# Optimization experiments

Hardware: AMD Instinct MI355X
Metric: run time of the kernel (lower is better)

Reference implementation:

```python
import jax, jax.numpy as jnp
import numpy as np
from jax import lax

V = 50000      # vocab_size; pad token id == V
E = 100        # embedding dim (hard-coded in module)
H = 512        # args.hidden
T = 200        # hard-coded sequence length
B = 256        # batch
NUM_CLASSES = 5


def setup_inputs() -> dict:
    key = jax.random.key(0)
    ks = jax.random.split(key, 10)
    X = jax.random.randint(ks[0], (B, T), 0, V + 1)  # values in [0, V]; V is pad
    emb = jax.random.normal(ks[1], (V + 1, E), jnp.float32) * 0.02
    def lstm_params(k, din):
        k1, k2, k3 = jax.random.split(k, 3)
        W_ih = jax.random.normal(k1, (4 * H, din), jnp.float32) * (1.0 / np.sqrt(din))
        W_hh = jax.random.normal(k2, (4 * H, H), jnp.float32) * (1.0 / np.sqrt(H))
        b = jax.random.uniform(k3, (4 * H,), jnp.float32, -0.05, 0.05)  # b_ih+b_hh fused
        return W_ih, W_hh, b
    W_ih0, W_hh0, b0 = lstm_params(ks[2], E)
    W_ih1, W_hh1, b1 = lstm_params(ks[3], H)
    W_out = jax.random.normal(ks[4], (NUM_CLASSES, H), jnp.float32) * (1.0 / np.sqrt(H))
    b_out = jnp.zeros((NUM_CLASSES,), jnp.float32)
    return {"X": X, "emb": emb, "W_ih0": W_ih0, "W_hh0": W_hh0, "b0": b0,
            "W_ih1": W_ih1, "W_hh1": W_hh1, "b1": b1, "W_out": W_out, "b_out": b_out}


def _lstm_layer(xs, W_ih, W_hh, b):
    # xs: [T, B, din] time-major; PyTorch gate order i, f, g, o
    Bsz = xs.shape[1]
    h0 = jnp.zeros((Bsz, H), xs.dtype)
    c0 = jnp.zeros((Bsz, H), xs.dtype)
    def step(carry, x_t):
        h, c = carry
        g = x_t @ W_ih.T + h @ W_hh.T + b          # [B, 4H]
        i, f, gg, o = jnp.split(g, 4, axis=-1)
        c = jax.nn.sigmoid(f) * c + jax.nn.sigmoid(i) * jnp.tanh(gg)
        h = jax.nn.sigmoid(o) * jnp.tanh(c)
        return (h, c), h
    (_, _), hs = lax.scan(step, (h0, c0), xs)
    return hs  # [T, B, H]


def reference(X, emb, W_ih0, W_hh0, b0, W_ih1, W_hh1, b1, W_out, b_out):
    x = emb[X]                                    # [B, T, E]
    xs = jnp.swapaxes(x, 0, 1)                    # [T, B, E] time-major
    hs = _lstm_layer(xs, W_ih0, W_hh0, b0)        # [T, B, H]
    hs = _lstm_layer(hs, W_ih1, W_hh1, b1)        # [T, B, H]
    out_seq = jnp.swapaxes(hs, 0, 1)              # [B, T, H]
    # last non-pad position per row (scan-from-end in the torch loop)
    pos = jnp.arange(T)
    nonpad = X != V                               # [B, T]
    last = jnp.max(jnp.where(nonpad, pos[None, :], -1), axis=1)  # [B]
    valid = pos[None, :] <= last[:, None]         # positions 0..last inclusive
    # take_output == 'maxpooling': max over output[:, :last+1, :]
    neg = jnp.finfo(out_seq.dtype).min
    pooled = jnp.max(jnp.where(valid[:, :, None], out_seq, neg), axis=1)  # [B, H]
    logits = pooled @ W_out.T + b_out             # [B, 5]
    return logits
```

## Files before the change

kernel.cpp:

```cpp
#include <hip/hip_runtime.h>
#include <float.h>

#define V 50000
#define E 100
#define H 512
#define T 200
#define B 256
#define NC 5
#define K0 640
#define K1 1024
#define NH (B * H)
#define NW0 (2048 * K0)
#define NW1 (2048 * K1)
#define LOSC 4096.0f
#define ILOSC (1.0f / 4096.0f)

typedef _Float16 half8 __attribute__((ext_vector_type(8)));
typedef float floatx4 __attribute__((ext_vector_type(4)));

__device__ __forceinline__ float fsig(float x)  { return 1.f / (1.f + __expf(-x)); }
__device__ __forceinline__ float ftanh(float x) { return 1.f - 2.f / (__expf(2.f * x) + 1.f); }

struct WS {
    _Float16 *W0h, *W0l, *W1h, *W1l;
    _Float16 *h0h, *h0l, *h1h, *h1l;
    float *c0, *c1, *hmax;
    int *last;
};
__device__ __host__ inline WS wsmap(char* p) {
    WS w;
    w.W0h = (_Float16*)p;  p += (size_t)NW0 * 2;
    w.W0l = (_Float16*)p;  p += (size_t)NW0 * 2;
    w.W1h = (_Float16*)p;  p += (size_t)NW1 * 2;
    w.W1l = (_Float16*)p;  p += (size_t)NW1 * 2;
    w.h0h = (_Float16*)p;  p += (size_t)2 * NH * 2;
    w.h0l = (_Float16*)p;  p += (size_t)2 * NH * 2;
    w.h1h = (_Float16*)p;  p += (size_t)2 * NH * 2;
    w.h1l = (_Float16*)p;  p += (size_t)2 * NH * 2;
    w.c0   = (float*)p;    p += (size_t)NH * 4;
    w.c1   = (float*)p;    p += (size_t)NH * 4;
    w.hmax = (float*)p;    p += (size_t)NH * 4;
    w.last = (int*)p;
    return w;
}

__global__ void k_prep(const float* __restrict__ Wih0, const float* __restrict__ Whh0,
                       const float* __restrict__ Wih1, const float* __restrict__ Whh1,
                       char* wsraw) {
    WS w = wsmap(wsraw);
    int idx = blockIdx.x * 256 + threadIdx.x;
    if (idx < NW0) {
        int c = idx / K0, k = idx - c * K0;
        int jx = c >> 2, g = c & 3, row = g * H + jx;
        float v = 0.f;
        if (k < 128) { if (k < E) v = Wih0[(size_t)row * E + k]; }
        else           v = Whh0[(size_t)row * H + (k - 128)];
        _Float16 hh = (_Float16)v;
        w.W0h[idx] = hh;
        w.W0l[idx] = (_Float16)((v - (float)hh) * LOSC);
    } else if (idx < NW0 + NW1) {
        int i2 = idx - NW0;
        int c = i2 / K1, k = i2 - c * K1;
        int jx = c >> 2, g = c & 3, row = g * H + jx;
        float v = (k < H) ? Wih1[(size_t)row * H + k]
                          : Whh1[(size_t)row * H + (k - H)];
        _Float16 hh = (_Float16)v;
        w.W1h[i2] = hh;
        w.W1l[i2] = (_Float16)((v - (float)hh) * LOSC);
    }
}

__global__ void k_init(const int* __restrict__ X, char* wsraw) {
    WS w = wsmap(wsraw);
    int i = blockIdx.x * 256 + threadIdx.x;
    if (i < 524288)                     ((unsigned*)w.h0h)[i] = 0u;
    else if (i < 524288 + 262144)       ((unsigned*)w.c0)[i - 524288] = 0u;
    else if (i < 524288 + 262144 + NH)  w.hmax[i - 786432] = -FLT_MAX;
    if (i < B) {
        int l = -1;
        const int* xr = X + i * T;
        for (int t = 0; t < T; ++t) if (xr[t] != V) l = t;
        w.last[i] = l;
    }
}

template <int LAYER>
__device__ __forceinline__ void run_mm(
    int t, const int* __restrict__ X, const float* __restrict__ emb,
    const _Float16* __restrict__ Wh, const _Float16* __restrict__ Wl,
    const _Float16* __restrict__ xh0, const _Float16* __restrict__ xl0,
    const _Float16* __restrict__ xh1, const _Float16* __restrict__ xl1,
    int c0g, int b0gl, int m, int qq, int wq,
    floatx4 (&acc0)[16], floatx4 (&acc1)[16])
{
    const int KT  = LAYER ? K1 : K0;
    const int NKB = LAYER ? 8 : 5;
    int erow[4];
    if (LAYER == 0) {
#pragma unroll
        for (int bs = 0; bs < 4; ++bs)
            erow[bs] = X[(b0gl + bs * 16 + m) * T + t];
    }
    half8 A_h[2][4], A_l[2][4], B_h[2][4], B_l[2][4];

    auto ldkb = [&](int kb, int buf) {
        const int ko = kb * 32 + qq * 8;
#pragma unroll
        for (int cs = 0; cs < 4; ++cs) {
            const size_t ro = (size_t)(c0g + cs * 16 + m) * KT + ko;
            A_h[buf][cs] = *(const half8*)(Wh + ro);
            A_l[buf][cs] = *(const half8*)(Wl + ro);
        }
        if (LAYER == 0 && kb < 4) {
#pragma unroll
            for (int bs = 0; bs < 4; ++bs) {
                const float* er = emb + (size_t)erow[bs] * E;
                float4 fa = make_float4(0.f,0.f,0.f,0.f), fb = fa;
                if (ko <= 96) fa = *(const float4*)(er + ko);
                if (ko <= 92) fb = *(const float4*)(er + ko + 4);
                float e[8] = {fa.x,fa.y,fa.z,fa.w, fb.x,fb.y,fb.z,fb.w};
                half8 hh, hl;
#pragma unroll
                for (int u = 0; u < 8; ++u) {
                    _Float16 hv = (_Float16)e[u];
                    hh[u] = hv;
                    hl[u] = (_Float16)((e[u] - (float)hv) * LOSC);
                }
                B_h[buf][bs] = hh; B_l[buf][bs] = hl;
            }
        } else {
            const _Float16 *sh, *sl; int kk;
            if (LAYER == 0)      { sh = xh0; sl = xl0; kk = ko - 128; }
            else if (kb < 16)    { sh = xh0; sl = xl0; kk = ko; }
            else                 { sh = xh1; sl = xl1; kk = ko - 512; }
#pragma unroll
            for (int bs = 0; bs < 4; ++bs) {
                const size_t ro = (size_t)(b0gl + bs * 16 + m) * H + kk;
                B_h[buf][bs] = *(const half8*)(sh + ro);
                B_l[buf][bs] = *(const half8*)(sl + ro);
            }
        }
    };

    ldkb(wq, 0);
#pragma unroll
    for (int i = 0; i < NKB; ++i) {
        const int cur = i & 1;
        if (i + 1 < NKB) ldkb(wq + 4 * (i + 1), cur ^ 1);
#pragma unroll
        for (int cs = 0; cs < 4; ++cs)
#pragma unroll
            for (int bs = 0; bs < 4; ++bs) {
                const int ti = cs * 4 + bs;
                acc0[ti] = __builtin_amdgcn_mfma_f32_16x16x32_f16(A_h[cur][cs], B_h[cur][bs], acc0[ti], 0, 0, 0);
                acc1[ti] = __builtin_amdgcn_mfma_f32_16x16x32_f16(A_h[cur][cs], B_l[cur][bs], acc1[ti], 0, 0, 0);
                acc1[ti] = __builtin_amdgcn_mfma_f32_16x16x32_f16(A_l[cur][cs], B_h[cur][bs], acc1[ti], 0, 0, 0);
            }
    }
}

__global__ __launch_bounds__(256, 1) void k_step(
    int t, const int* __restrict__ X, const float* __restrict__ emb,
    const float* __restrict__ b0, const float* __restrict__ b1,
    char* __restrict__ wsraw)
{
    extern __shared__ float red[];

    const int tid = threadIdx.x, lane = tid & 63, wq = tid >> 6;
    const int m = lane & 15, qq = lane >> 4;
    const int bid = blockIdx.x;
    const int xcd = bid & 7, slot = bid >> 3;
    const int layer = slot >> 4, bblk = (slot >> 2) & 3, chi = slot & 3;
    const int cblk = chi * 8 + xcd;
    if (layer == 0 && t >= T) return;
    if (layer == 1 && t < 1)  return;
    const int tt = t - 1;
    const int c0g = cblk * 64, b0gl = bblk * 64, j0g = cblk * 16;

    WS w = wsmap(wsraw);

    floatx4 acc0[16], acc1[16];
#pragma unroll
    for (int i = 0; i < 16; ++i) {
        floatx4 z = {0.f, 0.f, 0.f, 0.f};
        acc0[i] = z; acc1[i] = z;
    }

    if (layer == 0)
        run_mm<0>(t, X, emb, w.W0h, w.W0l,
                  w.h0h + (size_t)((t + 1) & 1) * NH, w.h0l + (size_t)((t + 1) & 1) * NH,
                  nullptr, nullptr, c0g, b0gl, m, qq, wq, acc0, acc1);
    else
        run_mm<1>(tt, X, emb, w.W1h, w.W1l,
                  w.h0h + (size_t)(tt & 1) * NH, w.h0l + (size_t)(tt & 1) * NH,
                  w.h1h + (size_t)((tt + 1) & 1) * NH, w.h1l + (size_t)((tt + 1) & 1) * NH,
                  c0g, b0gl, m, qq, wq, acc0, acc1);

#pragma unroll
    for (int cs = 0; cs < 4; ++cs)
#pragma unroll
        for (int bs = 0; bs < 4; ++bs) {
            floatx4 v = acc0[cs * 4 + bs] + acc1[cs * 4 + bs] * ILOSC;
            const int bl = bs * 16 + m, cl = cs * 16 + qq * 4;
            *(floatx4*)&red[((wq * 64 + bl) * 68 + cl)] = v;
        }
    __syncthreads();

    const int jj = lane & 15, bq = lane >> 4;
    const int j = j0g + jj;
    const float* bias = layer ? b1 : b0;
    const float bv0 = bias[0 * H + j], bv1 = bias[1 * H + j];
    const float bv2 = bias[2 * H + j], bv3 = bias[3 * H + j];
    float* cst = layer ? w.c1 : w.c0;
    _Float16* oh = layer ? (w.h1h + (size_t)(tt & 1) * NH) : (w.h0h + (size_t)(t & 1) * NH);
    _Float16* ol = layer ? (w.h1l + (size_t)(tt & 1) * NH) : (w.h0l + (size_t)(t & 1) * NH);

#pragma unroll
    for (int bi = 0; bi < 4; ++bi) {
        const int bl = wq * 16 + bq + 4 * bi;
        const int bg = b0gl + bl;
        floatx4 g = *(floatx4*)&red[((0 * 64 + bl) * 68 + jj * 4)];
#pragma unroll
        for (int q2 = 1; q2 < 4; ++q2)
            g += *(floatx4*)&red[((q2 * 64 + bl) * 68 + jj * 4)];
        float ig = fsig (g.x + bv0);
        float fg = fsig (g.y + bv1);
        float gg = ftanh(g.z + bv2);
        float og = fsig (g.w + bv3);
        float cold = cst[(size_t)bg * H + j];
        float cn = fg * cold + ig * gg;
        float hn = og * ftanh(cn);
        cst[(size_t)bg * H + j] = cn;
        _Float16 hh = (_Float16)hn;
        oh[(size_t)bg * H + j] = hh;
        ol[(size_t)bg * H + j] = (_Float16)((hn - (float)hh) * LOSC);
        if (layer == 1 && tt <= w.last[bg]) {
            float* hp = w.hmax + (size_t)bg * H + j;
            *hp = fmaxf(*hp, hn);
        }
    }
}

__global__ __launch_bounds__(64) void k_out(const float* __restrict__ hmax,
                                            const float* __restrict__ Wout,
                                            const float* __restrict__ bout,
                                            float* __restrict__ out) {
    const int b = blockIdx.x * 64 + threadIdx.x;
    float a[NC] = {0.f, 0.f, 0.f, 0.f, 0.f};
    const float* hm = hmax + (size_t)b * H;
    for (int j = 0; j < H; ++j) {
        float hv = hm[j];
#pragma unroll
        for (int cls = 0; cls < NC; ++cls)
            a[cls] = fmaf(hv, Wout[cls * H + j], a[cls]);
    }
#pragma unroll
    for (int cls = 0; cls < NC; ++cls)
        out[b * NC + cls] = a[cls] + bout[cls];
}

extern "C" void kernel_launch(void* const* d_in, const int* in_sizes, int n_in,
                              void* d_out, int out_size, void* d_ws, size_t ws_size,
                              hipStream_t stream) {
    const int*   X    = (const int*)  d_in[0];
    const float* emb  = (const float*)d_in[1];
    const float* Wih0 = (const float*)d_in[2];
    const float* Whh0 = (const float*)d_in[3];
    const float* b0   = (const float*)d_in[4];
    const float* Wih1 = (const float*)d_in[5];
    const float* Whh1 = (const float*)d_in[6];
    const float* b1   = (const float*)d_in[7];
    const float* Wout = (const float*)d_in[8];
    const float* bout = (const float*)d_in[9];
    float* out = (float*)d_out;
    char* ws = (char*)d_ws;
    WS w = wsmap(ws);

    k_prep<<<(NW0 + NW1 + 255) / 256, 256, 0, stream>>>(Wih0, Whh0, Wih1, Whh1, ws);
    k_init<<<(524288 + 262144 + NH + 255) / 256, 256, 0, stream>>>(X, ws);

    for (int t = 0; t <= T; ++t) {
        k_step<<<256, 256, 4 * 64 * 68 * sizeof(float), stream>>>(t, X, emb, b0, b1, ws);
    }

    k_out<<<4, 64, 0, stream>>>(w.hmax, Wout, bout, out);
}
```

Baseline: 4.895 ms.

## Fuse per-timestep launches into one persistent cooperative kernel with grid barrier

```diff
diff --git a/kernel.cpp b/kernel.cpp
--- a/kernel.cpp
+++ b/kernel.cpp
@@ -14,6 +14,7 @@
 #define NW1 (2048 * K1)
 #define LOSC 4096.0f
 #define ILOSC (1.0f / 4096.0f)
+#define NBLK 256
 
 typedef _Float16 half8 __attribute__((ext_vector_type(8)));
 typedef float floatx4 __attribute__((ext_vector_type(4)));
@@ -26,6 +27,7 @@
     _Float16 *h0h, *h0l, *h1h, *h1l;
     float *c0, *c1, *hmax;
     int *last;
+    unsigned *bar;
 };
 __device__ __host__ inline WS wsmap(char* p) {
     WS w;
@@ -40,7 +42,8 @@
     w.c0   = (float*)p;    p += (size_t)NH * 4;
     w.c1   = (float*)p;    p += (size_t)NH * 4;
     w.hmax = (float*)p;    p += (size_t)NH * 4;
-    w.last = (int*)p;
+    w.last = (int*)p;      p += (size_t)B * 4;
+    w.bar  = (unsigned*)p;
     return w;
 }
 
@@ -73,15 +76,26 @@
 __global__ void k_init(const int* __restrict__ X, char* wsraw) {
     WS w = wsmap(wsraw);
     int i = blockIdx.x * 256 + threadIdx.x;
-    if (i < 524288)                     ((unsigned*)w.h0h)[i] = 0u;
-    else if (i < 524288 + 262144)       ((unsigned*)w.c0)[i - 524288] = 0u;
-    else if (i < 524288 + 262144 + NH)  w.hmax[i - 786432] = -FLT_MAX;
+    if (i < 524288) ((unsigned*)w.h0h)[i] = 0u;
     if (i < B) {
         int l = -1;
         const int* xr = X + i * T;
         for (int t = 0; t < T; ++t) if (xr[t] != V) l = t;
         w.last[i] = l;
     }
+    if (i == 0) *w.bar = 0u;
+}
+
+__device__ __forceinline__ void grid_sync(unsigned* cnt, unsigned target) {
+    __syncthreads();
+    if (threadIdx.x == 0) {
+        __threadfence();
+        __hip_atomic_fetch_add(cnt, 1u, __ATOMIC_RELAXED, __HIP_MEMORY_SCOPE_AGENT);
+        while (__hip_atomic_load(cnt, __ATOMIC_RELAXED, __HIP_MEMORY_SCOPE_AGENT) < target)
+            __builtin_amdgcn_s_sleep(1);
+        __threadfence();
+    }
+    __syncthreads();
 }
 
 template <int LAYER>
@@ -159,8 +173,8 @@
     }
 }
 
-__global__ __launch_bounds__(256, 1) void k_step(
-    int t, const int* __restrict__ X, const float* __restrict__ emb,
+__global__ __launch_bounds__(256, 1) void k_lstm(
+    const int* __restrict__ X, const float* __restrict__ emb,
     const float* __restrict__ b0, const float* __restrict__ b1,
     char* __restrict__ wsraw)
 {
@@ -172,71 +186,89 @@
     const int xcd = bid & 7, slot = bid >> 3;
     const int layer = slot >> 4, bblk = (slot >> 2) & 3, chi = slot & 3;
     const int cblk = chi * 8 + xcd;
-    if (layer == 0 && t >= T) return;
-    if (layer == 1 && t < 1)  return;
-    const int tt = t - 1;
     const int c0g = cblk * 64, b0gl = bblk * 64, j0g = cblk * 16;
 
     WS w = wsmap(wsraw);
-
-    floatx4 acc0[16], acc1[16];
-#pragma unroll
-    for (int i = 0; i < 16; ++i) {
-        floatx4 z = {0.f, 0.f, 0.f, 0.f};
-        acc0[i] = z; acc1[i] = z;
-    }
-
-    if (layer == 0)
-        run_mm<0>(t, X, emb, w.W0h, w.W0l,
-                  w.h0h + (size_t)((t + 1) & 1) * NH, w.h0l + (size_t)((t + 1) & 1) * NH,
-                  nullptr, nullptr, c0g, b0gl, m, qq, wq, acc0, acc1);
-    else
-        run_mm<1>(tt, X, emb, w.W1h, w.W1l,
-                  w.h0h + (size_t)(tt & 1) * NH, w.h0l + (size_t)(tt & 1) * NH,
-                  w.h1h + (size_t)((tt + 1) & 1) * NH, w.h1l + (size_t)((tt + 1) & 1) * NH,
-                  c0g, b0gl, m, qq, wq, acc0, acc1);
-
-#pragma unroll
-    for (int cs = 0; cs < 4; ++cs)
-#pragma unroll
-        for (int bs = 0; bs < 4; ++bs) {
-            floatx4 v = acc0[cs * 4 + bs] + acc1[cs * 4 + bs] * ILOSC;
-            const int bl = bs * 16 + m, cl = cs * 16 + qq * 4;
-            *(floatx4*)&red[((wq * 64 + bl) * 68 + cl)] = v;
-        }
-    __syncthreads();
 
     const int jj = lane & 15, bq = lane >> 4;
     const int j = j0g + jj;
     const float* bias = layer ? b1 : b0;
     const float bv0 = bias[0 * H + j], bv1 = bias[1 * H + j];
     const float bv2 = bias[2 * H + j], bv3 = bias[3 * H + j];
-    float* cst = layer ? w.c1 : w.c0;
-    _Float16* oh = layer ? (w.h1h + (size_t)(tt & 1) * NH) : (w.h0h + (size_t)(t & 1) * NH);
-    _Float16* ol = layer ? (w.h1l + (size_t)(tt & 1) * NH) : (w.h0l + (size_t)(t & 1) * NH);
-
+
+    float creg[4], hmreg[4];
+    int lastr[4];
 #pragma unroll
     for (int bi = 0; bi < 4; ++bi) {
-        const int bl = wq * 16 + bq + 4 * bi;
-        const int bg = b0gl + bl;
-        floatx4 g = *(floatx4*)&red[((0 * 64 + bl) * 68 + jj * 4)];
-#pragma unroll
-        for (int q2 = 1; q2 < 4; ++q2)
-            g += *(floatx4*)&red[((q2 * 64 + bl) * 68 + jj * 4)];
-        float ig = fsig (g.x + bv0);
-        float fg = fsig (g.y + bv1);
-        float gg = ftanh(g.z + bv2);
-        float og = fsig (g.w + bv3);
-        float cold = cst[(size_t)bg * H + j];
-        float cn = fg * cold + ig * gg;
-        float hn = og * ftanh(cn);
-        cst[(size_t)bg * H + j] = cn;
-        _Float16 hh = (_Float16)hn;
-        oh[(size_t)bg * H + j] = hh;
-        ol[(size_t)bg * H + j] = (_Float16)((hn - (float)hh) * LOSC);
-        if (layer == 1 && tt <= w.last[bg]) {
-            float* hp = w.hmax + (size_t)bg * H + j;
-            *hp = fmaxf(*hp, hn);
+        creg[bi]  = 0.f;
+        hmreg[bi] = -FLT_MAX;
+        lastr[bi] = w.last[b0gl + wq * 16 + bq + 4 * bi];
+    }
+
+    for (int t = 0; t <= T; ++t) {
+        const int tt = t - 1;
+        const bool act = layer ? (t >= 1) : (t < T);
+        if (act) {
+            floatx4 acc0[16], acc1[16];
+#pragma unroll
+            for (int i = 0; i < 16; ++i) {
+                floatx4 z = {0.f, 0.f, 0.f, 0.f};
+                acc0[i] = z; acc1[i] = z;
+            }
+
+            if (layer == 0)
+                run_mm<0>(t, X, emb, w.W0h, w.W0l,
+                          w.h0h + (size_t)((t + 1) & 1) * NH, w.h0l + (size_t)((t + 1) & 1) * NH,
+                          nullptr, nullptr, c0g, b0gl, m, qq, wq, acc0, acc1);
+            else
+                run_mm<1>(tt, X, emb, w.W1h, w.W1l,
+                          w.h0h + (size_t)(tt & 1) * NH, w.h0l + (size_t)(tt & 1) * NH,
+                          w.h1h + (size_t)((tt + 1) & 1) * NH, w.h1l + (size_t)((tt + 1) & 1) * NH,
+                          c0g, b0gl, m, qq, wq, acc0, acc1);
+
+#pragma unroll
+            for (int cs = 0; cs < 4; ++cs)
+#pragma unroll
+                for (int bs = 0; bs < 4; ++bs) {
+                    floatx4 v = acc0[cs * 4 + bs] + acc1[cs * 4 + bs] * ILOSC;
+                    const int bl = bs * 16 + m, cl = cs * 16 + qq * 4;
+                    *(floatx4*)&red[((wq * 64 + bl) * 68 + cl)] = v;
+                }
+            __syncthreads();
+
+            _Float16 *oh, *ol;
+            if (layer == 0) { oh = w.h0h + (size_t)(t  & 1) * NH; ol = w.h0l + (size_t)(t  & 1) * NH; }
+            else            { oh = w.h1h + (size_t)(tt & 1) * NH; ol = w.h1l + (size_t)(tt & 1) * NH; }
+
+#pragma unroll
+            for (int bi = 0; bi < 4; ++bi) {
+                const int bl = wq * 16 + bq + 4 * bi;
+                const int bg = b0gl + bl;
+                floatx4 g = *(floatx4*)&red[((0 * 64 + bl) * 68 + jj * 4)];
+#pragma unroll
+                for (int q2 = 1; q2 < 4; ++q2)
+                    g += *(floatx4*)&red[((q2 * 64 + bl) * 68 + jj * 4)];
+                float ig = fsig (g.x + bv0);
+                float fg = fsig (g.y + bv1);
+                float gg = ftanh(g.z + bv2);
+                float og = fsig (g.w + bv3);
+                float cn = fg * creg[bi] + ig * gg;
+                float hn = og * ftanh(cn);
+                creg[bi] = cn;
+                _Float16 hh = (_Float16)hn;
+                oh[(size_t)bg * H + j] = hh;
+                ol[(size_t)bg * H + j] = (_Float16)((hn - (float)hh) * LOSC);
+                if (layer == 1 && tt <= lastr[bi]) hmreg[bi] = fmaxf(hmreg[bi], hn);
+            }
+        }
+        if (t < T) grid_sync(w.bar, (unsigned)(t + 1) * NBLK);
+    }
+
+    if (layer == 1) {
+#pragma unroll
+        for (int bi = 0; bi < 4; ++bi) {
+            const int bg = b0gl + wq * 16 + bq + 4 * bi;
+            w.hmax[(size_t)bg * H + j] = hmreg[bi];
         }
     }
 }
@@ -277,10 +309,16 @@
     WS w = wsmap(ws);
 
     k_prep<<<(NW0 + NW1 + 255) / 256, 256, 0, stream>>>(Wih0, Whh0, Wih1, Whh1, ws);
-    k_init<<<(524288 + 262144 + NH + 255) / 256, 256, 0, stream>>>(X, ws);
-
-    for (int t = 0; t <= T; ++t) {
-        k_step<<<256, 256, 4 * 64 * 68 * sizeof(float), stream>>>(t, X, emb, b0, b1, ws);
+    k_init<<<2048, 256, 0, stream>>>(X, ws);
+
+    {
+        const unsigned smem = (unsigned)(4 * 64 * 68 * sizeof(float));
+        void* args[] = {(void*)&X, (void*)&emb, (void*)&b0, (void*)&b1, (void*)&ws};
+        hipError_t e = hipLaunchCooperativeKernel((const void*)k_lstm, dim3(NBLK), dim3(256),
+                                                  args, smem, stream);
+        if (e != hipSuccess) {
+            k_lstm<<<NBLK, 256, smem, stream>>>(X, emb, b0, b1, ws);
+        }
     }
 
     k_out<<<4, 64, 0, stream>>>(w.hmax, Wout, bout, out);
```

Measured after the change: 9.466 ms. 1.93x slower.
